# Optimization experiments

Measured on AMD Instinct MI355X. Metric: run time of the kernel, lower is better.

Reference implementation:

```python
import jax, jax.numpy as jnp
import numpy as np

B, T, D, H = 16, 1024, 768, 64

def setup_inputs() -> dict:
    key = jax.random.key(0)
    k1, k2, k3, k4 = jax.random.split(key, 4)
    scale = 0.02
    x = jax.random.normal(k1, (B, T, D), dtype=jnp.float32)
    Wq = jax.random.normal(k2, (H, D), dtype=jnp.float32) * scale
    Wk = jax.random.normal(k3, (H, D), dtype=jnp.float32) * scale
    Wv = jax.random.normal(k4, (H, D), dtype=jnp.float32) * scale
    return {"x": x, "Wq": Wq, "Wk": Wk, "Wv": Wv}

def reference(x, Wq, Wk, Wv):
    # q,k,v: [B,T,H]  (nn.Linear with no bias: x @ W^T)
    q = jnp.einsum('btd,hd->bth', x, Wq)
    k = jnp.einsum('btd,hd->bth', x, Wk)
    v = jnp.einsum('btd,hd->bth', x, Wv)
    T_ = x.shape[1]
    # NOTE: original scales by emb_dim**-0.5 (not head_size**-0.5)
    scores = jnp.einsum('bth,bsh->bts', q, k) * (x.shape[-1] ** -0.5)
    causal = jnp.tril(jnp.ones((T_, T_), dtype=bool))
    scores = jnp.where(causal, scores, -jnp.inf)
    attn = jax.nn.softmax(scores, axis=-1)
    return jnp.einsum('bts,bsh->bth', attn, v)
```

## Files before the change

### kernel.cpp

```cpp
#include <hip/hip_runtime.h>
#include <hip/hip_bf16.h>

typedef __attribute__((ext_vector_type(8))) short bf16x8;
typedef __attribute__((ext_vector_type(4))) float f32x4;

#define BATCH 16
#define SEQ   1024
#define EMB   768
#define HEAD  64
#define NT    (BATCH*SEQ)
#define NQKV  192

__device__ inline ushort f2bf(float f) {
  __hip_bfloat16 h = __float2bfloat16(f);
  return *reinterpret_cast<const ushort*>(&h);
}

__device__ inline void lds_dma16(const void* g, void* l) {
  __builtin_amdgcn_global_load_lds(
      (const __attribute__((address_space(1))) void*)g,
      (__attribute__((address_space(3))) void*)l, 16, 0, 0);
}

__global__ __launch_bounds__(256) void convw_kernel(
    const float* __restrict__ Wq, const float* __restrict__ Wk,
    const float* __restrict__ Wv, ushort* __restrict__ wt)
{
  const int row = blockIdx.x * 8 + (threadIdx.x >> 5);
  const float* W = (row < 64) ? Wq : (row < 128 ? Wk : Wv);
  const int r = row & 63;
  #pragma unroll
  for (int j = 0; j < 3; ++j) {
    const int c = (threadIdx.x & 31) + 32 * j;
    const int grp = c >> 3, gst = c & 7;
    const int glog = gst ^ (row & 7);
    const int srccol = (grp << 6) + (glog << 3);
    const float4 f0 = *reinterpret_cast<const float4*>(&W[(size_t)r * EMB + srccol]);
    const float4 f1 = *reinterpret_cast<const float4*>(&W[(size_t)r * EMB + srccol + 4]);
    union { ushort us[8]; uint4 u; } o;
    o.us[0]=f2bf(f0.x); o.us[1]=f2bf(f0.y); o.us[2]=f2bf(f0.z); o.us[3]=f2bf(f0.w);
    o.us[4]=f2bf(f1.x); o.us[5]=f2bf(f1.y); o.us[6]=f2bf(f1.z); o.us[7]=f2bf(f1.w);
    *reinterpret_cast<uint4*>(&wt[(size_t)row * EMB + (c << 3)]) = o.u;
  }
}

__global__ __launch_bounds__(256) void proj_kernel(
    const float* __restrict__ x, const ushort* __restrict__ wt,
    ushort* __restrict__ qo, ushort* __restrict__ ko, ushort* __restrict__ vo)
{
  __shared__ ushort Xl[2][32 * 64];
  __shared__ ushort Wl[2][96 * 64];

  const int tid  = threadIdx.x;
  const int wave = tid >> 6, lane = tid & 63;
  const int m0   = (blockIdx.x >> 1) * 32;
  const int nb96 = (blockIdx.x & 1) * 96;
  const int wr   = wave >> 1, wc = wave & 1;
  const int col16 = lane & 15, quad = lane >> 4;

  const int xrow = tid >> 3;
  const int xchk = tid & 7;

  float4 xa, xb;

  #define LOADX(kt_) {                                                          \
    const float* p = &x[(size_t)(m0 + xrow) * EMB + (kt_) * 64 + xchk * 8];     \
    xa = *reinterpret_cast<const float4*>(p);                                   \
    xb = *reinterpret_cast<const float4*>(p + 4); }

  #define WRITEX(buf_) {                                                        \
    union { ushort us[8]; uint4 u; } p;                                         \
    p.us[0]=f2bf(xa.x); p.us[1]=f2bf(xa.y); p.us[2]=f2bf(xa.z); p.us[3]=f2bf(xa.w); \
    p.us[4]=f2bf(xb.x); p.us[5]=f2bf(xb.y); p.us[6]=f2bf(xb.z); p.us[7]=f2bf(xb.w); \
    *reinterpret_cast<uint4*>(&Xl[buf_][xrow * 64 + ((xchk ^ (xrow & 7)) << 3)]) = p.u; }

  #define STAGEW(kt_, buf_) { _Pragma("unroll")                                 \
    for (int u = 0; u < 3; ++u) {                                               \
      lds_dma16(&wt[(size_t)(nb96 + u * 32 + wave * 8 + (lane >> 3)) * EMB + (kt_) * 64 + (lane & 7) * 8], \
                &Wl[buf_][(u * 32 + wave * 8) * 64]);                           \
    } }

  f32x4 acc[3];
  #pragma unroll
  for (int n = 0; n < 3; ++n) acc[n] = (f32x4){0.f, 0.f, 0.f, 0.f};

  LOADX(0); STAGEW(0, 0); WRITEX(0);

  int cur = 0;
  for (int kt = 0; kt < 12; ++kt) {
    __syncthreads();
    if (kt < 11) { LOADX(kt + 1); STAGEW(kt + 1, cur ^ 1); }
    #pragma unroll
    for (int ks = 0; ks < 2; ++ks) {
      const int g = ks * 4 + quad;
      const int ar = wr * 16 + col16;
      const bf16x8 a = *reinterpret_cast<const bf16x8*>(
          &Xl[cur][ar * 64 + ((g ^ (ar & 7)) << 3)]);
      #pragma unroll
      for (int n = 0; n < 3; ++n) {
        const int br = wc * 48 + 16 * n + col16;
        const bf16x8 b = *reinterpret_cast<const bf16x8*>(
            &Wl[cur][br * 64 + ((g ^ (br & 7)) << 3)]);
        acc[n] = __builtin_amdgcn_mfma_f32_16x16x32_bf16(a, b, acc[n], 0, 0, 0);
      }
    }
    if (kt < 11) WRITEX(cur ^ 1);
    cur ^= 1;
  }

  #pragma unroll
  for (int n = 0; n < 3; ++n) {
    const int c   = nb96 + wc * 48 + 16 * n + col16;
    const int sel = c >> 6, h = c & 63;
    #pragma unroll
    for (int i = 0; i < 4; ++i) {
      const int t = m0 + wr * 16 + quad * 4 + i;
      const ushort val = f2bf(acc[n][i]);
      if (sel == 0) {
        qo[(size_t)t * HEAD + h] = val;
      } else if (sel == 1) {
        const int hs = (((h >> 3) ^ (t & 7)) << 3) | (h & 7);
        ko[(size_t)t * HEAD + hs] = val;
      } else {
        const int bb = t >> 10, tin = t & 1023;
        const int ts = (tin & ~63) | (((((tin >> 3) & 7) ^ (h & 7))) << 3) | (tin & 7);
        vo[((size_t)bb * HEAD + h) * SEQ + ts] = val;
      }
    }
  }
  #undef LOADX
  #undef WRITEX
  #undef STAGEW
}

__global__ __launch_bounds__(256) void attn_kernel(
    const ushort* __restrict__ q, const ushort* __restrict__ k,
    const ushort* __restrict__ vT, float* __restrict__ out)
{
  __shared__ ushort Kl[2][64 * 64];
  __shared__ ushort Vl[2][64 * 64];
  __shared__ ushort lp[4][16][72];

  const int tid  = threadIdx.x;
  const int wave = tid >> 6, lane = tid & 63;
  const int bid  = blockIdx.x;
  const int b    = bid & 15;
  const int j    = 15 - (bid >> 4);
  const int qt0  = j * 64;
  const int nt   = j + 1;
  const float SC2 = 0.03608439182435161f * 1.4426950408889634f;

  const int col  = lane & 15;
  const int quad = lane >> 4;
  const int koff = quad * 8;

  const size_t qb = ((size_t)b * SEQ + qt0 + 16 * wave + col) * HEAD;
  const bf16x8 qa0 = *reinterpret_cast<const bf16x8*>(&q[qb + koff]);
  const bf16x8 qa1 = *reinterpret_cast<const bf16x8*>(&q[qb + koff + 32]);

  #define STAGE(t_, buf_) {                                                     \
    _Pragma("unroll")                                                           \
    for (int r = 0; r < 2; ++r)                                                 \
      lds_dma16(&k[((size_t)b * SEQ + (t_) * 64 + r * 32 + wave * 8 + (lane >> 3)) * HEAD + (lane & 7) * 8], \
                &Kl[buf_][(r * 32 + wave * 8) * 64]);                           \
    _Pragma("unroll")                                                           \
    for (int r = 0; r < 2; ++r)                                                 \
      lds_dma16(&vT[((size_t)b * HEAD + r * 32 + wave * 8 + (lane >> 3)) * SEQ + (t_) * 64 + (lane & 7) * 8], \
                &Vl[buf_][(r * 32 + wave * 8) * 64]);                           \
  }

  f32x4 o[4];
  #pragma unroll
  for (int hf = 0; hf < 4; ++hf) o[hf] = (f32x4){0.f, 0.f, 0.f, 0.f};
  float l_part[4];
  #pragma unroll
  for (int i = 0; i < 4; ++i) l_part[i] = 0.f;

  STAGE(0, 0);

  for (int t = 0; t < nt; ++t) {
    const int cur = t & 1;
    __syncthreads();
    if (t + 1 < nt) STAGE(t + 1, cur ^ 1);

    f32x4 s[4];
    #pragma unroll
    for (int f = 0; f < 4; ++f) {
      const int rowf = 16 * f + col;
      const bf16x8 kb0 = *reinterpret_cast<const bf16x8*>(
          &Kl[cur][rowf * 64 + ((quad ^ (rowf & 7)) << 3)]);
      const bf16x8 kb1 = *reinterpret_cast<const bf16x8*>(
          &Kl[cur][rowf * 64 + (((quad + 4) ^ (rowf & 7)) << 3)]);
      f32x4 z = (f32x4){0.f, 0.f, 0.f, 0.f};
      z    = __builtin_amdgcn_mfma_f32_16x16x32_bf16(qa0, kb0, z, 0, 0, 0);
      s[f] = __builtin_amdgcn_mfma_f32_16x16x32_bf16(qa1, kb1, z, 0, 0, 0);
    }

    const bool last = (t == nt - 1);
    #pragma unroll
    for (int f = 0; f < 4; ++f) {
      const int kvc = t * 64 + 16 * f + col;
      #pragma unroll
      for (int i = 0; i < 4; ++i) {
        float v = s[f][i];
        if (last && kvc > qt0 + 16 * wave + quad * 4 + i) v = -1e30f;
        const float p = exp2f(v * SC2);
        l_part[i] += p;
        lp[wave][quad * 4 + i][16 * f + col] = f2bf(p);
      }
    }

    #pragma unroll
    for (int ks = 0; ks < 2; ++ks) {
      const bf16x8 pa = *reinterpret_cast<const bf16x8*>(&lp[wave][col][ks * 32 + koff]);
      #pragma unroll
      for (int hf = 0; hf < 4; ++hf) {
        const int vrow = 16 * hf + col;
        const int g = ks * 4 + quad;
        const bf16x8 vb = *reinterpret_cast<const bf16x8*>(
            &Vl[cur][vrow * 64 + ((g ^ (vrow & 7)) << 3)]);
        o[hf] = __builtin_amdgcn_mfma_f32_16x16x32_bf16(pa, vb, o[hf], 0, 0, 0);
      }
    }
  }

  #pragma unroll
  for (int i = 0; i < 4; ++i) {
    #pragma unroll
    for (int d = 1; d < 16; d <<= 1) l_part[i] += __shfl_xor(l_part[i], d);
  }
  #pragma unroll
  for (int i = 0; i < 4; ++i) {
    const float inv = 1.0f / l_part[i];
    const int tq = qt0 + 16 * wave + quad * 4 + i;
    #pragma unroll
    for (int hf = 0; hf < 4; ++hf)
      out[((size_t)b * SEQ + tq) * HEAD + 16 * hf + col] = o[hf][i] * inv;
  }
  #undef STAGE
}

extern "C" void kernel_launch(void* const* d_in, const int* in_sizes, int n_in,
                              void* d_out, int out_size, void* d_ws, size_t ws_size,
                              hipStream_t stream) {
  const float* x  = (const float*)d_in[0];
  const float* Wq = (const float*)d_in[1];
  const float* Wk = (const float*)d_in[2];
  const float* Wv = (const float*)d_in[3];

  ushort* qw  = (ushort*)d_ws;
  ushort* kw  = qw + (size_t)NT * HEAD;
  ushort* vTw = kw + (size_t)NT * HEAD;
  ushort* wtw = vTw + (size_t)NT * HEAD;
  float*  out = (float*)d_out;

  convw_kernel<<<NQKV / 8, 256, 0, stream>>>(Wq, Wk, Wv, wtw);
  proj_kernel<<<(NT / 32) * 2, 256, 0, stream>>>(x, wtw, qw, kw, vTw);
  attn_kernel<<<BATCH * (SEQ / 64), 256, 0, stream>>>(qw, kw, vTw, out);
}
```

Measured before the change: 50.14 us.

## Split long causal attention tiles across two blocks and enlarge projection tiles

The attention kernel now splits the KV range of the eight longest query tiles per batch into two halves handled by separate blocks. Each half writes unnormalized partial outputs and row sums, and a new combine kernel merges them. This is meant to even out the causal work imbalance and fill more CUs. The projection kernel moves to 512-thread blocks that each compute 64 rows across all 192 output columns, which removes the duplicate x loads and conversions of the previous 2-way column split. The cost is extra partial-output traffic plus one more kernel launch.

```diff
diff --git a/kernel.cpp b/kernel.cpp
--- a/kernel.cpp
+++ b/kernel.cpp
@@ -44,29 +44,28 @@
   }
 }
 
-__global__ __launch_bounds__(256) void proj_kernel(
+__global__ __launch_bounds__(512, 4) void proj_kernel(
     const float* __restrict__ x, const ushort* __restrict__ wt,
     ushort* __restrict__ qo, ushort* __restrict__ ko, ushort* __restrict__ vo)
 {
-  __shared__ ushort Xl[2][32 * 64];
-  __shared__ ushort Wl[2][96 * 64];
+  __shared__ ushort Xl[2][64 * 64];
+  __shared__ ushort Wl[2][192 * 64];
 
   const int tid  = threadIdx.x;
   const int wave = tid >> 6, lane = tid & 63;
-  const int m0   = (blockIdx.x >> 1) * 32;
-  const int nb96 = (blockIdx.x & 1) * 96;
-  const int wr   = wave >> 1, wc = wave & 1;
+  const int m0   = blockIdx.x * 64;
+  const int wr   = wave >> 2, wc = wave & 3;
   const int col16 = lane & 15, quad = lane >> 4;
 
   const int xrow = tid >> 3;
+  const int xc   = (tid & 7) * 8;
   const int xchk = tid & 7;
 
   float4 xa, xb;
 
   #define LOADX(kt_) {                                                          \
-    const float* p = &x[(size_t)(m0 + xrow) * EMB + (kt_) * 64 + xchk * 8];     \
-    xa = *reinterpret_cast<const float4*>(p);                                   \
-    xb = *reinterpret_cast<const float4*>(p + 4); }
+    xa = *reinterpret_cast<const float4*>(&x[(size_t)(m0 + xrow) * EMB + (kt_) * 64 + xc]);     \
+    xb = *reinterpret_cast<const float4*>(&x[(size_t)(m0 + xrow) * EMB + (kt_) * 64 + xc + 4]); }
 
   #define WRITEX(buf_) {                                                        \
     union { ushort us[8]; uint4 u; } p;                                         \
@@ -76,13 +75,15 @@
 
   #define STAGEW(kt_, buf_) { _Pragma("unroll")                                 \
     for (int u = 0; u < 3; ++u) {                                               \
-      lds_dma16(&wt[(size_t)(nb96 + u * 32 + wave * 8 + (lane >> 3)) * EMB + (kt_) * 64 + (lane & 7) * 8], \
-                &Wl[buf_][(u * 32 + wave * 8) * 64]);                           \
+      lds_dma16(&wt[(size_t)(u * 64 + (tid >> 3)) * EMB + (kt_) * 64 + (tid & 7) * 8], \
+                &Wl[buf_][(u * 64 + wave * 8) * 64]);                           \
     } }
 
-  f32x4 acc[3];
-  #pragma unroll
-  for (int n = 0; n < 3; ++n) acc[n] = (f32x4){0.f, 0.f, 0.f, 0.f};
+  f32x4 acc[2][3];
+  #pragma unroll
+  for (int m = 0; m < 2; ++m)
+    #pragma unroll
+    for (int n = 0; n < 3; ++n) acc[m][n] = (f32x4){0.f, 0.f, 0.f, 0.f};
 
   LOADX(0); STAGEW(0, 0); WRITEX(0);
 
@@ -93,15 +94,19 @@
     #pragma unroll
     for (int ks = 0; ks < 2; ++ks) {
       const int g = ks * 4 + quad;
-      const int ar = wr * 16 + col16;
-      const bf16x8 a = *reinterpret_cast<const bf16x8*>(
-          &Xl[cur][ar * 64 + ((g ^ (ar & 7)) << 3)]);
+      bf16x8 a[2];
+      #pragma unroll
+      for (int m = 0; m < 2; ++m) {
+        const int ar = wr * 32 + 16 * m + col16;
+        a[m] = *reinterpret_cast<const bf16x8*>(&Xl[cur][ar * 64 + ((g ^ (ar & 7)) << 3)]);
+      }
       #pragma unroll
       for (int n = 0; n < 3; ++n) {
         const int br = wc * 48 + 16 * n + col16;
-        const bf16x8 b = *reinterpret_cast<const bf16x8*>(
-            &Wl[cur][br * 64 + ((g ^ (br & 7)) << 3)]);
-        acc[n] = __builtin_amdgcn_mfma_f32_16x16x32_bf16(a, b, acc[n], 0, 0, 0);
+        const bf16x8 b = *reinterpret_cast<const bf16x8*>(&Wl[cur][br * 64 + ((g ^ (br & 7)) << 3)]);
+        #pragma unroll
+        for (int m = 0; m < 2; ++m)
+          acc[m][n] = __builtin_amdgcn_mfma_f32_16x16x32_bf16(a[m], b, acc[m][n], 0, 0, 0);
       }
     }
     if (kt < 11) WRITEX(cur ^ 1);
@@ -110,21 +115,24 @@
 
   #pragma unroll
   for (int n = 0; n < 3; ++n) {
-    const int c   = nb96 + wc * 48 + 16 * n + col16;
+    const int c   = wc * 48 + 16 * n + col16;
     const int sel = c >> 6, h = c & 63;
     #pragma unroll
-    for (int i = 0; i < 4; ++i) {
-      const int t = m0 + wr * 16 + quad * 4 + i;
-      const ushort val = f2bf(acc[n][i]);
-      if (sel == 0) {
-        qo[(size_t)t * HEAD + h] = val;
-      } else if (sel == 1) {
-        const int hs = (((h >> 3) ^ (t & 7)) << 3) | (h & 7);
-        ko[(size_t)t * HEAD + hs] = val;
-      } else {
-        const int bb = t >> 10, tin = t & 1023;
-        const int ts = (tin & ~63) | (((((tin >> 3) & 7) ^ (h & 7))) << 3) | (tin & 7);
-        vo[((size_t)bb * HEAD + h) * SEQ + ts] = val;
+    for (int m = 0; m < 2; ++m) {
+      #pragma unroll
+      for (int i = 0; i < 4; ++i) {
+        const int t = m0 + wr * 32 + 16 * m + quad * 4 + i;
+        const ushort val = f2bf(acc[m][n][i]);
+        if (sel == 0) {
+          qo[(size_t)t * HEAD + h] = val;
+        } else if (sel == 1) {
+          const int hs = (((h >> 3) ^ (t & 7)) << 3) | (h & 7);
+          ko[(size_t)t * HEAD + hs] = val;
+        } else {
+          const int bb = t >> 10, tin = t & 1023;
+          const int ts = (tin & ~63) | (((((tin >> 3) & 7) ^ (h & 7))) << 3) | (tin & 7);
+          vo[((size_t)bb * HEAD + h) * SEQ + ts] = val;
+        }
       }
     }
   }
@@ -135,7 +143,8 @@
 
 __global__ __launch_bounds__(256) void attn_kernel(
     const ushort* __restrict__ q, const ushort* __restrict__ k,
-    const ushort* __restrict__ vT, float* __restrict__ out)
+    const ushort* __restrict__ vT, float* __restrict__ out,
+    float* __restrict__ po, float* __restrict__ pl)
 {
   __shared__ ushort Kl[2][64 * 64];
   __shared__ ushort Vl[2][64 * 64];
@@ -144,10 +153,16 @@
   const int tid  = threadIdx.x;
   const int wave = tid >> 6, lane = tid & 63;
   const int bid  = blockIdx.x;
-  const int b    = bid & 15;
-  const int j    = 15 - (bid >> 4);
-  const int qt0  = j * 64;
-  const int nt   = j + 1;
+
+  int b, j, s, nsplit;
+  if (bid < 256) { b = bid & 15; const int u = bid >> 4; j = 8 + (u >> 1); s = u & 1; nsplit = 2; }
+  else           { const int v = bid - 256; b = v & 15; j = 7 - (v >> 4); s = 0; nsplit = 1; }
+
+  const int qt0 = j * 64;
+  const int nt  = j + 1;
+  const int h2  = (nt + 1) >> 1;
+  const int t0  = (nsplit == 2 && s == 1) ? h2 : 0;
+  const int t1  = (nsplit == 2 && s == 0) ? h2 : nt;
   const float SC2 = 0.03608439182435161f * 1.4426950408889634f;
 
   const int col  = lane & 15;
@@ -176,14 +191,14 @@
   #pragma unroll
   for (int i = 0; i < 4; ++i) l_part[i] = 0.f;
 
-  STAGE(0, 0);
-
-  for (int t = 0; t < nt; ++t) {
-    const int cur = t & 1;
+  STAGE(t0, 0);
+
+  for (int t = t0; t < t1; ++t) {
+    const int cur = (t - t0) & 1;
     __syncthreads();
-    if (t + 1 < nt) STAGE(t + 1, cur ^ 1);
-
-    f32x4 s[4];
+    if (t + 1 < t1) STAGE(t + 1, cur ^ 1);
+
+    f32x4 sreg[4];
     #pragma unroll
     for (int f = 0; f < 4; ++f) {
       const int rowf = 16 * f + col;
@@ -192,8 +207,8 @@
       const bf16x8 kb1 = *reinterpret_cast<const bf16x8*>(
           &Kl[cur][rowf * 64 + (((quad + 4) ^ (rowf & 7)) << 3)]);
       f32x4 z = (f32x4){0.f, 0.f, 0.f, 0.f};
-      z    = __builtin_amdgcn_mfma_f32_16x16x32_bf16(qa0, kb0, z, 0, 0, 0);
-      s[f] = __builtin_amdgcn_mfma_f32_16x16x32_bf16(qa1, kb1, z, 0, 0, 0);
+      z       = __builtin_amdgcn_mfma_f32_16x16x32_bf16(qa0, kb0, z, 0, 0, 0);
+      sreg[f] = __builtin_amdgcn_mfma_f32_16x16x32_bf16(qa1, kb1, z, 0, 0, 0);
     }
 
     const bool last = (t == nt - 1);
@@ -202,7 +217,7 @@
       const int kvc = t * 64 + 16 * f + col;
       #pragma unroll
       for (int i = 0; i < 4; ++i) {
-        float v = s[f][i];
+        float v = sreg[f][i];
         if (last && kvc > qt0 + 16 * wave + quad * 4 + i) v = -1e30f;
         const float p = exp2f(v * SC2);
         l_part[i] += p;
@@ -229,15 +244,44 @@
     #pragma unroll
     for (int d = 1; d < 16; d <<= 1) l_part[i] += __shfl_xor(l_part[i], d);
   }
-  #pragma unroll
-  for (int i = 0; i < 4; ++i) {
-    const float inv = 1.0f / l_part[i];
-    const int tq = qt0 + 16 * wave + quad * 4 + i;
-    #pragma unroll
-    for (int hf = 0; hf < 4; ++hf)
-      out[((size_t)b * SEQ + tq) * HEAD + 16 * hf + col] = o[hf][i] * inv;
+
+  if (nsplit == 1) {
+    #pragma unroll
+    for (int i = 0; i < 4; ++i) {
+      const float inv = 1.0f / l_part[i];
+      const int tq = qt0 + 16 * wave + quad * 4 + i;
+      #pragma unroll
+      for (int hf = 0; hf < 4; ++hf)
+        out[((size_t)b * SEQ + tq) * HEAD + 16 * hf + col] = o[hf][i] * inv;
+    }
+  } else {
+    const int pidx = (b * 8 + (j - 8)) * 2 + s;
+    float* pob = &po[(size_t)pidx * 4096];
+    #pragma unroll
+    for (int i = 0; i < 4; ++i) {
+      const int r = 16 * wave + quad * 4 + i;
+      #pragma unroll
+      for (int hf = 0; hf < 4; ++hf)
+        pob[r * 64 + 16 * hf + col] = o[hf][i];
+      if (col == 0) pl[pidx * 64 + r] = l_part[i];
+    }
   }
   #undef STAGE
+}
+
+__global__ __launch_bounds__(256) void combine_kernel(
+    const float* __restrict__ po, const float* __restrict__ pl,
+    float* __restrict__ out)
+{
+  const int idx = blockIdx.x * 256 + threadIdx.x;
+  const int c  = idx & 63;
+  const int r  = (idx >> 6) & 63;
+  const int jj = (idx >> 12) & 7;
+  const int b  = idx >> 15;
+  const int p0 = (b * 8 + jj) * 2;
+  const float num = po[(size_t)p0 * 4096 + r * 64 + c] + po[(size_t)(p0 + 1) * 4096 + r * 64 + c];
+  const float den = pl[p0 * 64 + r] + pl[(p0 + 1) * 64 + r];
+  out[((size_t)b * SEQ + (jj + 8) * 64 + r) * HEAD + c] = num / den;
 }
 
 extern "C" void kernel_launch(void* const* d_in, const int* in_sizes, int n_in,
@@ -248,13 +292,17 @@
   const float* Wk = (const float*)d_in[2];
   const float* Wv = (const float*)d_in[3];
 
-  ushort* qw  = (ushort*)d_ws;
-  ushort* kw  = qw + (size_t)NT * HEAD;
-  ushort* vTw = kw + (size_t)NT * HEAD;
-  ushort* wtw = vTw + (size_t)NT * HEAD;
+  char* base = (char*)d_ws;
+  ushort* qw  = (ushort*)(base);
+  ushort* kw  = (ushort*)(base + (2u << 20));
+  ushort* vTw = (ushort*)(base + (4u << 20));
+  ushort* wtw = (ushort*)(base + (6u << 20));
+  float*  po  = (float*) (base + (8u << 20));
+  float*  pl  = (float*) (base + (12u << 20));
   float*  out = (float*)d_out;
 
   convw_kernel<<<NQKV / 8, 256, 0, stream>>>(Wq, Wk, Wv, wtw);
-  proj_kernel<<<(NT / 32) * 2, 256, 0, stream>>>(x, wtw, qw, kw, vTw);
-  attn_kernel<<<BATCH * (SEQ / 64), 256, 0, stream>>>(qw, kw, vTw, out);
-}
+  proj_kernel<<<NT / 64, 512, 0, stream>>>(x, wtw, qw, kw, vTw);
+  attn_kernel<<<384, 256, 0, stream>>>(qw, kw, vTw, out, po, pl);
+  combine_kernel<<<2048, 256, 0, stream>>>(po, pl, out);
+}
```

After: 44.04 us. 1.14x faster.
